# Kernel optimization log

Hardware: AMD Instinct MI355X
Metric: run time of the kernel (lower is better)

Reference implementation:

```python
import jax, jax.numpy as jnp
import numpy as np

B, S, F = 1024, 48, 16          # batch, time steps, features (D = S*F = 768)
N = 100000                       # training corpus size


def setup_inputs() -> dict:
    key = jax.random.key(0)
    k1, k2, k3 = jax.random.split(key, 3)
    x = jax.random.normal(k1, (B, S, F), dtype=jnp.float32)
    X_train = jax.random.normal(k2, (N, S * F), dtype=jnp.float32)
    Y_train = jax.random.normal(k3, (N, 24, 1), dtype=jnp.float32)
    return {"x": x, "X_train": X_train, "Y_train": Y_train}


def reference(x, X_train, Y_train):
    # Flatten queries: [B, 48*F]
    x_flat = x.reshape(x.shape[0], -1)
    # Euclidean cdist via ||a||^2 + ||b||^2 - 2 a.b (matches torch.cdist p=2)
    q2 = jnp.sum(x_flat * x_flat, axis=1, keepdims=True)        # [B, 1]
    t2 = jnp.sum(X_train * X_train, axis=1)[None, :]            # [1, N]
    cross = jnp.einsum('bd,nd->bn', x_flat, X_train)            # [B, N]
    d2 = jnp.maximum(q2 + t2 - 2.0 * cross, 0.0)
    distances = jnp.sqrt(d2)                                     # [B, N]
    nearest = jnp.argmin(distances, axis=1)                      # [B]
    y_pred = Y_train[nearest]                                    # [B, 24, 1]
    return y_pred
```

## Files before the change

### kernel.cpp

```cpp
#include <hip/hip_runtime.h>

#define N_TRAIN 100000
#define DIM 768
#define NQ 1024
#define BN 48
#define NCHUNK 2084
#define MARGIN 6.0f
#define MAXC 65536

typedef __bf16 bf16x8 __attribute__((ext_vector_type(8)));
typedef float f32x4 __attribute__((ext_vector_type(4)));
typedef unsigned short u16x8 __attribute__((ext_vector_type(8)));

__device__ __forceinline__ unsigned short f2bf(float f) {
  unsigned int u = __builtin_bit_cast(unsigned int, f);
  u = (u + 0x7FFFu + ((u >> 16) & 1u)) >> 16;
  return (unsigned short)u;
}
__device__ __forceinline__ float bf2f(unsigned short h) {
  return __builtin_bit_cast(float, (unsigned int)h << 16);
}
__device__ __forceinline__ unsigned int fenc(float f) {
  unsigned int u = __builtin_bit_cast(unsigned int, f);
  return (u & 0x80000000u) ? ~u : (u | 0x80000000u);
}
__device__ __forceinline__ float fdec(unsigned int u) {
  u = (u & 0x80000000u) ? (u & 0x7FFFFFFFu) : ~u;
  return __builtin_bit_cast(float, u);
}

__global__ void initK(unsigned long long* res, unsigned int* gmin, unsigned int* cnt) {
  int t = threadIdx.x;
  res[t] = ~0ull;
  gmin[t] = 0xFFFFFFFFu;
  if (t == 0) *cnt = 0u;
}

__global__ void convA(const float* __restrict__ x, unsigned short* __restrict__ Asw) {
  int t = blockIdx.x * 256 + threadIdx.x;
  int l = t & 63;
  int fragid = t >> 6;
  int mf = fragid / 24;
  int ks = fragid - mf * 24;
  int row = mf * 16 + (l & 15);
  int k = ks * 32 + (l >> 4) * 8;
  const float* src = x + (size_t)row * DIM + k;
  u16x8 h;
#pragma unroll
  for (int i = 0; i < 8; ++i) h[i] = f2bf(src[i]);
  *(u16x8*)(Asw + (size_t)fragid * 512 + l * 8) = h;
}

__global__ __launch_bounds__(512, 4) void passA(
    const float* __restrict__ Xt, const unsigned short* __restrict__ Asw,
    float* __restrict__ bmin, int fine) {
  __shared__ __align__(16) unsigned short Bs[BN * DIM];
  __shared__ float t2p[BN][8];
  __shared__ float t2s[BN];
  const int tid = threadIdx.x;
  const int chunk = blockIdx.x;

  if (tid < 384) {
    const int c = tid >> 3;
    const int sl = tid & 7;
    const int n = chunk * BN + c;
    float ss = 0.f;
    if (n < N_TRAIN) {
      const float* src = Xt + (size_t)n * DIM + sl * 8;
#pragma unroll
      for (int j = 0; j < 12; ++j) {
        f32x4 v0 = *(const f32x4*)(src + j * 64);
        f32x4 v1 = *(const f32x4*)(src + j * 64 + 4);
        u16x8 h;
        h[0] = f2bf(v0[0]); h[1] = f2bf(v0[1]); h[2] = f2bf(v0[2]); h[3] = f2bf(v0[3]);
        h[4] = f2bf(v1[0]); h[5] = f2bf(v1[1]); h[6] = f2bf(v1[2]); h[7] = f2bf(v1[3]);
#pragma unroll
        for (int i = 0; i < 8; ++i) { float f = bf2f(h[i]); ss = fmaf(f, f, ss); }
        int e = (c * DIM + sl * 8 + j * 64) ^ ((c & 7) << 3);
        *(u16x8*)(&Bs[e]) = h;
      }
    } else {
      u16x8 h;
#pragma unroll
      for (int i = 0; i < 8; ++i) h[i] = 0;
#pragma unroll
      for (int j = 0; j < 12; ++j) {
        int e = (c * DIM + sl * 8 + j * 64) ^ ((c & 7) << 3);
        *(u16x8*)(&Bs[e]) = h;
      }
    }
    t2p[c][sl] = ss;
  }
  __syncthreads();
  if (tid < BN) {
    float s = 0.f;
#pragma unroll
    for (int j = 0; j < 8; ++j) s += t2p[tid][j];
    t2s[tid] = (chunk * BN + tid < N_TRAIN) ? s : 3.0e38f;
  }
  __syncthreads();

  const int wid = tid >> 6;
  const int l = tid & 63;
  const int lc = l & 15;
  const int lg = l >> 4;

  for (int mt = 0; mt < 2; ++mt) {
    f32x4 acc[4][3];
#pragma unroll
    for (int rf = 0; rf < 4; ++rf)
#pragma unroll
      for (int cf = 0; cf < 3; ++cf) {
        acc[rf][cf][0] = 0.f; acc[rf][cf][1] = 0.f;
        acc[rf][cf][2] = 0.f; acc[rf][cf][3] = 0.f;
      }
    const int mfbase = mt * 32 + wid * 4;
    for (int ks = 0; ks < 24; ++ks) {
      bf16x8 a[4], b[3];
#pragma unroll
      for (int rf = 0; rf < 4; ++rf)
        a[rf] = __builtin_bit_cast(bf16x8,
                  *(const u16x8*)(Asw + (size_t)((mfbase + rf) * 24 + ks) * 512 + l * 8));
#pragma unroll
      for (int cf = 0; cf < 3; ++cf) {
        int col = cf * 16 + lc;
        int idx = (col * DIM + ks * 32 + lg * 8) ^ ((col & 7) << 3);
        b[cf] = __builtin_bit_cast(bf16x8, *(const u16x8*)(&Bs[idx]));
      }
#pragma unroll
      for (int rf = 0; rf < 4; ++rf)
#pragma unroll
        for (int cf = 0; cf < 3; ++cf)
          acc[rf][cf] = __builtin_amdgcn_mfma_f32_16x16x32_bf16(a[rf], b[cf], acc[rf][cf], 0, 0, 0);
    }
    const int rowbase = mt * 512 + wid * 64;
#pragma unroll
    for (int rf = 0; rf < 4; ++rf) {
#pragma unroll
      for (int reg = 0; reg < 4; ++reg) {
        int row = rowbase + rf * 16 + lg * 4 + reg;
        if (fine) {
#pragma unroll
          for (int cf = 0; cf < 3; ++cf) {
            float v = t2s[cf * 16 + lc] - 2.f * acc[rf][cf][reg];
#pragma unroll
            for (int s = 1; s < 16; s <<= 1) v = fminf(v, __shfl_xor(v, s));
            if (lc == 0)
              bmin[(size_t)chunk * (NQ * 3) + row * 3 + cf] = v;
          }
        } else {
          float v = 3.0e38f;
#pragma unroll
          for (int cf = 0; cf < 3; ++cf)
            v = fminf(v, t2s[cf * 16 + lc] - 2.f * acc[rf][cf][reg]);
#pragma unroll
          for (int s = 1; s < 16; s <<= 1) v = fminf(v, __shfl_xor(v, s));
          if (lc == 0)
            bmin[(size_t)chunk * NQ + row] = v;
        }
      }
    }
  }
}

__global__ __launch_bounds__(256) void passB1(const float* __restrict__ bmin,
                                              unsigned int* __restrict__ gmin, int bpq) {
  int qg = blockIdx.x >> 4, cs = blockIdx.x & 15;
  int w = threadIdx.x >> 6, l = threadIdx.x & 63;
  int q = qg * 64 + l;
  float m = 3.0e38f;
  for (int j = cs * 4 + w; j < NCHUNK; j += 64) {
    const float* p = bmin + (size_t)j * (NQ * bpq) + q * bpq;
    for (int cf = 0; cf < bpq; ++cf) m = fminf(m, p[cf]);
  }
  __shared__ float sm[4][64];
  sm[w][l] = m;
  __syncthreads();
  if (threadIdx.x < 64) {
    float v = fminf(fminf(sm[0][l], sm[1][l]), fminf(sm[2][l], sm[3][l]));
    atomicMin(&gmin[q], fenc(v));
  }
}

__global__ __launch_bounds__(256) void passB2(const float* __restrict__ bmin,
                                              const unsigned int* __restrict__ gmin,
                                              unsigned int* __restrict__ cnt,
                                              unsigned int* __restrict__ cand, int bpq) {
  int qg = blockIdx.x >> 4, cs = blockIdx.x & 15;
  int w = threadIdx.x >> 6, l = threadIdx.x & 63;
  int q = qg * 64 + l;
  float thr = fdec(gmin[q]) + MARGIN;
  for (int j = cs * 4 + w; j < NCHUNK; j += 64) {
    const float* p = bmin + (size_t)j * (NQ * bpq) + q * bpq;
    for (int cf = 0; cf < bpq; ++cf) {
      if (p[cf] <= thr) {
        unsigned int pos = atomicAdd(cnt, 1u);
        if (pos < MAXC) cand[pos] = ((unsigned int)q << 16) | (unsigned int)(j * bpq + cf);
      }
    }
  }
}

__global__ void passC(const float* __restrict__ x, const float* __restrict__ Xt,
                      const unsigned int* __restrict__ cnt, const unsigned int* __restrict__ cand,
                      unsigned long long* __restrict__ res, int cpbsh, int ncols) {
  unsigned int count = *cnt;
  if (count > MAXC) count = MAXC;
  int w = threadIdx.x >> 6, l = threadIdx.x & 63;
  long pairs = (long)count << cpbsh;
  for (long p = (long)blockIdx.x * 4 + w; p < pairs; p += (long)gridDim.x * 4) {
    unsigned int cd = cand[p >> cpbsh];
    int q = cd >> 16;
    int blk = cd & 0xFFFF;
    int col = (int)(p & ((1 << cpbsh) - 1));
    int n = blk * ncols + col;
    if (col >= ncols || n >= N_TRAIN) continue;
    const float* xq = x + (size_t)q * DIM;
    const float* tn = Xt + (size_t)n * DIM;
    float s = 0.f;
#pragma unroll
    for (int i = 0; i < 12; ++i) {
      float d = xq[i * 64 + l] - tn[i * 64 + l];
      s = fmaf(d, d, s);
    }
#pragma unroll
    for (int sh = 1; sh < 64; sh <<= 1) s += __shfl_xor(s, sh);
    if (l == 0) {
      unsigned long long key =
          ((unsigned long long)__builtin_bit_cast(unsigned int, s) << 32) | (unsigned int)n;
      atomicMin(res + q, key);
    }
  }
}

__global__ void passD(const unsigned long long* __restrict__ res,
                      const float* __restrict__ Y, float* __restrict__ out) {
  int t = blockIdx.x * 256 + threadIdx.x;
  if (t < NQ * 24) {
    int q = t / 24, j = t - q * 24;
    unsigned int idx = (unsigned int)(res[q] & 0xFFFFFFFFu);
    out[t] = Y[(size_t)idx * 24 + j];
  }
}

extern "C" void kernel_launch(void* const* d_in, const int* in_sizes, int n_in,
                              void* d_out, int out_size, void* d_ws, size_t ws_size,
                              hipStream_t stream) {
  const float* x  = (const float*)d_in[0];
  const float* Xt = (const float*)d_in[1];
  const float* Y  = (const float*)d_in[2];
  float* out = (float*)d_out;
  char* ws = (char*)d_ws;
  unsigned long long* res  = (unsigned long long*)(ws);
  unsigned int*       cnt  = (unsigned int*)(ws + 8192);
  unsigned int*       gmin = (unsigned int*)(ws + 8448);
  unsigned int*       cand = (unsigned int*)(ws + 12544);
  unsigned short*     Asw  = (unsigned short*)(ws + 274688);
  float*              bmin = (float*)(ws + 1847552);

  size_t needFine = 1847552ull + (size_t)NCHUNK * NQ * 3 * 4ull;
  int fine, bpq, cpbsh, ncols;
  if (ws_size >= needFine) { fine = 1; bpq = 3; cpbsh = 4; ncols = 16; }
  else                     { fine = 0; bpq = 1; cpbsh = 6; ncols = 48; }

  hipLaunchKernelGGL(initK,  dim3(1),      dim3(1024), 0, stream, res, gmin, cnt);
  hipLaunchKernelGGL(convA,  dim3(384),    dim3(256),  0, stream, x, Asw);
  hipLaunchKernelGGL(passA,  dim3(NCHUNK), dim3(512),  0, stream, Xt, Asw, bmin, fine);
  hipLaunchKernelGGL(passB1, dim3(256),    dim3(256),  0, stream, bmin, gmin, bpq);
  hipLaunchKernelGGL(passB2, dim3(256),    dim3(256),  0, stream, bmin, gmin, cnt, cand, bpq);
  hipLaunchKernelGGL(passC,  dim3(512),    dim3(256),  0, stream, x, Xt, cnt, cand, res, cpbsh, ncols);
  hipLaunchKernelGGL(passD,  dim3(96),     dim3(256),  0, stream, res, Y, out);
}
```

Measured before the change: 340.8 us.

## Switch coarse distance pass from bf16 to fp8 MFMA with wider chunks

The coarse screening GEMM now quantises queries and training rows to FP8 (E4M3) instead of bf16 and uses the fp8 16x16x32 MFMA, halving operand bytes in LDS and the A buffer. The chunk width doubles to 96 columns, with the warp tiling reshaped to 2x6 fragments. The candidate margin is widened to absorb the larger quantisation error, so the exact re-rank pass sees more candidates. The software fp8 conversion with rounding is heavier per element than the bf16 conversion, and the wider margin may inflate later passes.

```diff
diff --git a/kernel.cpp b/kernel.cpp
--- a/kernel.cpp
+++ b/kernel.cpp
@@ -3,22 +3,46 @@
 #define N_TRAIN 100000
 #define DIM 768
 #define NQ 1024
-#define BN 48
-#define NCHUNK 2084
-#define MARGIN 6.0f
+#define BN 96
+#define NCHUNK 1042
+#define MARGIN 36.0f
 #define MAXC 65536
 
-typedef __bf16 bf16x8 __attribute__((ext_vector_type(8)));
 typedef float f32x4 __attribute__((ext_vector_type(4)));
-typedef unsigned short u16x8 __attribute__((ext_vector_type(8)));
-
-__device__ __forceinline__ unsigned short f2bf(float f) {
+typedef unsigned long long u64;
+typedef u64 u64x2 __attribute__((ext_vector_type(2)));
+
+__device__ __forceinline__ unsigned char f2q(float f) {
   unsigned int u = __builtin_bit_cast(unsigned int, f);
-  u = (u + 0x7FFFu + ((u >> 16) & 1u)) >> 16;
-  return (unsigned short)u;
-}
-__device__ __forceinline__ float bf2f(unsigned short h) {
-  return __builtin_bit_cast(float, (unsigned int)h << 16);
+  unsigned int s = (u >> 24) & 0x80u;
+  int e = (int)((u >> 23) & 0xFFu) - 127;
+  unsigned int m = u & 0x7FFFFFu;
+  if (e < -9) return (unsigned char)s;
+  if (e < -6) {
+    int rb = 20 + (-6 - e);
+    unsigned int full = 0x800000u | m;
+    unsigned int q = full >> rb;
+    unsigned int rem = full & ((1u << rb) - 1u);
+    unsigned int half = 1u << (rb - 1);
+    q += (rem > half) || (rem == half && (q & 1u));
+    return (unsigned char)(s | q);
+  }
+  unsigned int q = m >> 20;
+  unsigned int rem = m & 0xFFFFFu;
+  q += (rem > 0x80000u) || (rem == 0x80000u && (q & 1u));
+  int ee = e + 7;
+  if (q == 8u) { q = 0u; ee += 1; }
+  if (ee >= 16) return (unsigned char)(s | 0x7Eu);
+  return (unsigned char)(s | ((unsigned)ee << 3) | q);
+}
+__device__ __forceinline__ float q2f(unsigned char h) {
+  unsigned int s = ((unsigned int)h & 0x80u) << 24;
+  int ee = (h >> 3) & 15; unsigned int m = h & 7u;
+  if (ee == 0) {
+    float v = (float)m * 0.001953125f;
+    return __builtin_bit_cast(float, s | __builtin_bit_cast(unsigned int, v));
+  }
+  return __builtin_bit_cast(float, s | ((unsigned int)(ee + 120) << 23) | (m << 20));
 }
 __device__ __forceinline__ unsigned int fenc(float f) {
   unsigned int u = __builtin_bit_cast(unsigned int, f);
@@ -36,7 +60,7 @@
   if (t == 0) *cnt = 0u;
 }
 
-__global__ void convA(const float* __restrict__ x, unsigned short* __restrict__ Asw) {
+__global__ void convA(const float* __restrict__ x, unsigned char* __restrict__ Asw) {
   int t = blockIdx.x * 256 + threadIdx.x;
   int l = t & 63;
   int fragid = t >> 6;
@@ -45,49 +69,55 @@
   int row = mf * 16 + (l & 15);
   int k = ks * 32 + (l >> 4) * 8;
   const float* src = x + (size_t)row * DIM + k;
-  u16x8 h;
-#pragma unroll
-  for (int i = 0; i < 8; ++i) h[i] = f2bf(src[i]);
-  *(u16x8*)(Asw + (size_t)fragid * 512 + l * 8) = h;
+  u64 v = 0;
+#pragma unroll
+  for (int i = 0; i < 8; ++i) v |= (u64)f2q(src[i]) << (8 * i);
+  *(u64*)(Asw + (size_t)fragid * 512 + l * 8) = v;
 }
 
 __global__ __launch_bounds__(512, 4) void passA(
-    const float* __restrict__ Xt, const unsigned short* __restrict__ Asw,
+    const float* __restrict__ Xt, const unsigned char* __restrict__ Asw,
     float* __restrict__ bmin, int fine) {
-  __shared__ __align__(16) unsigned short Bs[BN * DIM];
-  __shared__ float t2p[BN][8];
+  __shared__ __align__(16) unsigned char Bs[BN * DIM];
+  __shared__ float t2p[BN][16];
   __shared__ float t2s[BN];
   const int tid = threadIdx.x;
   const int chunk = blockIdx.x;
 
-  if (tid < 384) {
-    const int c = tid >> 3;
-    const int sl = tid & 7;
-    const int n = chunk * BN + c;
+  for (int i = 0; i < 3; ++i) {
+    int idx = tid + i * 512;
+    int c = idx >> 4, sl = idx & 15;
+    int n = chunk * BN + c;
+    int base = c * DIM + sl * 48;
+    int xm = (c & 15) << 4;
     float ss = 0.f;
     if (n < N_TRAIN) {
-      const float* src = Xt + (size_t)n * DIM + sl * 8;
-#pragma unroll
-      for (int j = 0; j < 12; ++j) {
-        f32x4 v0 = *(const f32x4*)(src + j * 64);
-        f32x4 v1 = *(const f32x4*)(src + j * 64 + 4);
-        u16x8 h;
-        h[0] = f2bf(v0[0]); h[1] = f2bf(v0[1]); h[2] = f2bf(v0[2]); h[3] = f2bf(v0[3]);
-        h[4] = f2bf(v1[0]); h[5] = f2bf(v1[1]); h[6] = f2bf(v1[2]); h[7] = f2bf(v1[3]);
-#pragma unroll
-        for (int i = 0; i < 8; ++i) { float f = bf2f(h[i]); ss = fmaf(f, f, ss); }
-        int e = (c * DIM + sl * 8 + j * 64) ^ ((c & 7) << 3);
-        *(u16x8*)(&Bs[e]) = h;
+      const float* src = Xt + (size_t)n * DIM + sl * 48;
+#pragma unroll
+      for (int j = 0; j < 3; ++j) {
+        f32x4 v0 = *(const f32x4*)(src + j * 16);
+        f32x4 v1 = *(const f32x4*)(src + j * 16 + 4);
+        f32x4 v2 = *(const f32x4*)(src + j * 16 + 8);
+        f32x4 v3 = *(const f32x4*)(src + j * 16 + 12);
+        u64 lo = 0, hi = 0;
+#pragma unroll
+        for (int k = 0; k < 4; ++k) {
+          unsigned char b0 = f2q(v0[k]); float d0 = q2f(b0); ss = fmaf(d0, d0, ss);
+          lo |= (u64)b0 << (8 * k);
+          unsigned char b1 = f2q(v1[k]); float d1 = q2f(b1); ss = fmaf(d1, d1, ss);
+          lo |= (u64)b1 << (8 * (k + 4));
+          unsigned char b2 = f2q(v2[k]); float d2 = q2f(b2); ss = fmaf(d2, d2, ss);
+          hi |= (u64)b2 << (8 * k);
+          unsigned char b3 = f2q(v3[k]); float d3 = q2f(b3); ss = fmaf(d3, d3, ss);
+          hi |= (u64)b3 << (8 * (k + 4));
+        }
+        u64x2 w; w[0] = lo; w[1] = hi;
+        *(u64x2*)(&Bs[(base + j * 16) ^ xm]) = w;
       }
     } else {
-      u16x8 h;
-#pragma unroll
-      for (int i = 0; i < 8; ++i) h[i] = 0;
-#pragma unroll
-      for (int j = 0; j < 12; ++j) {
-        int e = (c * DIM + sl * 8 + j * 64) ^ ((c & 7) << 3);
-        *(u16x8*)(&Bs[e]) = h;
-      }
+      u64x2 w; w[0] = 0; w[1] = 0;
+#pragma unroll
+      for (int j = 0; j < 3; ++j) *(u64x2*)(&Bs[(base + j * 16) ^ xm]) = w;
     }
     t2p[c][sl] = ss;
   }
@@ -95,7 +125,7 @@
   if (tid < BN) {
     float s = 0.f;
 #pragma unroll
-    for (int j = 0; j < 8; ++j) s += t2p[tid][j];
+    for (int j = 0; j < 16; ++j) s += t2p[tid][j];
     t2s[tid] = (chunk * BN + tid < N_TRAIN) ? s : 3.0e38f;
   }
   __syncthreads();
@@ -105,53 +135,59 @@
   const int lc = l & 15;
   const int lg = l >> 4;
 
-  for (int mt = 0; mt < 2; ++mt) {
-    f32x4 acc[4][3];
-#pragma unroll
-    for (int rf = 0; rf < 4; ++rf)
-#pragma unroll
-      for (int cf = 0; cf < 3; ++cf) {
+  int cb[6], xm[6];
+#pragma unroll
+  for (int cf = 0; cf < 6; ++cf) {
+    int c = cf * 16 + lc;
+    cb[cf] = c * DIM + lg * 8;
+    xm[cf] = (c & 15) << 4;
+  }
+
+  for (int mt = 0; mt < 4; ++mt) {
+    f32x4 acc[2][6];
+#pragma unroll
+    for (int rf = 0; rf < 2; ++rf)
+#pragma unroll
+      for (int cf = 0; cf < 6; ++cf) {
         acc[rf][cf][0] = 0.f; acc[rf][cf][1] = 0.f;
         acc[rf][cf][2] = 0.f; acc[rf][cf][3] = 0.f;
       }
-    const int mfbase = mt * 32 + wid * 4;
+    const int mfbase = mt * 16 + wid * 2;
+    const unsigned char* ap = Asw + (size_t)mfbase * 24 * 512 + l * 8;
+
     for (int ks = 0; ks < 24; ++ks) {
-      bf16x8 a[4], b[3];
-#pragma unroll
-      for (int rf = 0; rf < 4; ++rf)
-        a[rf] = __builtin_bit_cast(bf16x8,
-                  *(const u16x8*)(Asw + (size_t)((mfbase + rf) * 24 + ks) * 512 + l * 8));
-#pragma unroll
-      for (int cf = 0; cf < 3; ++cf) {
-        int col = cf * 16 + lc;
-        int idx = (col * DIM + ks * 32 + lg * 8) ^ ((col & 7) << 3);
-        b[cf] = __builtin_bit_cast(bf16x8, *(const u16x8*)(&Bs[idx]));
-      }
-#pragma unroll
-      for (int rf = 0; rf < 4; ++rf)
-#pragma unroll
-        for (int cf = 0; cf < 3; ++cf)
-          acc[rf][cf] = __builtin_amdgcn_mfma_f32_16x16x32_bf16(a[rf], b[cf], acc[rf][cf], 0, 0, 0);
-    }
-    const int rowbase = mt * 512 + wid * 64;
-#pragma unroll
-    for (int rf = 0; rf < 4; ++rf) {
+      long a0 = *(const long*)(ap + ks * 512);
+      long a1 = *(const long*)(ap + (24 + ks) * 512);
+      long b[6];
+#pragma unroll
+      for (int cf = 0; cf < 6; ++cf)
+        b[cf] = *(const long*)(&Bs[(cb[cf] + ks * 32) ^ xm[cf]]);
+#pragma unroll
+      for (int cf = 0; cf < 6; ++cf) {
+        acc[0][cf] = __builtin_amdgcn_mfma_f32_16x16x32_fp8_fp8(a0, b[cf], acc[0][cf], 0, 0, 0);
+        acc[1][cf] = __builtin_amdgcn_mfma_f32_16x16x32_fp8_fp8(a1, b[cf], acc[1][cf], 0, 0, 0);
+      }
+    }
+
+    const int rowbase = mt * 256 + wid * 32;
+#pragma unroll
+    for (int rf = 0; rf < 2; ++rf) {
 #pragma unroll
       for (int reg = 0; reg < 4; ++reg) {
         int row = rowbase + rf * 16 + lg * 4 + reg;
         if (fine) {
 #pragma unroll
-          for (int cf = 0; cf < 3; ++cf) {
+          for (int cf = 0; cf < 6; ++cf) {
             float v = t2s[cf * 16 + lc] - 2.f * acc[rf][cf][reg];
 #pragma unroll
             for (int s = 1; s < 16; s <<= 1) v = fminf(v, __shfl_xor(v, s));
             if (lc == 0)
-              bmin[(size_t)chunk * (NQ * 3) + row * 3 + cf] = v;
+              bmin[(size_t)chunk * (NQ * 6) + row * 6 + cf] = v;
           }
         } else {
           float v = 3.0e38f;
 #pragma unroll
-          for (int cf = 0; cf < 3; ++cf)
+          for (int cf = 0; cf < 6; ++cf)
             v = fminf(v, t2s[cf * 16 + lc] - 2.f * acc[rf][cf][reg]);
 #pragma unroll
           for (int s = 1; s < 16; s <<= 1) v = fminf(v, __shfl_xor(v, s));
@@ -255,13 +291,13 @@
   unsigned int*       cnt  = (unsigned int*)(ws + 8192);
   unsigned int*       gmin = (unsigned int*)(ws + 8448);
   unsigned int*       cand = (unsigned int*)(ws + 12544);
-  unsigned short*     Asw  = (unsigned short*)(ws + 274688);
-  float*              bmin = (float*)(ws + 1847552);
-
-  size_t needFine = 1847552ull + (size_t)NCHUNK * NQ * 3 * 4ull;
+  unsigned char*      Asw  = (unsigned char*)(ws + 274688);
+  float*              bmin = (float*)(ws + 1061120);
+
+  size_t needFine = 1061120ull + (size_t)NCHUNK * NQ * 6 * 4ull;
   int fine, bpq, cpbsh, ncols;
-  if (ws_size >= needFine) { fine = 1; bpq = 3; cpbsh = 4; ncols = 16; }
-  else                     { fine = 0; bpq = 1; cpbsh = 6; ncols = 48; }
+  if (ws_size >= needFine) { fine = 1; bpq = 6; cpbsh = 4; ncols = 16; }
+  else                     { fine = 0; bpq = 1; cpbsh = 7; ncols = 96; }
 
   hipLaunchKernelGGL(initK,  dim3(1),      dim3(1024), 0, stream, res, gmin, cnt);
   hipLaunchKernelGGL(convA,  dim3(384),    dim3(256),  0, stream, x, Asw);
```

Result: slower. 529.7 us (+55.4%).
